# Optimization experiments

Hardware: AMD Instinct MI355X
Metric: run time of the kernel (lower is better)

## Reference

```python
import jax, jax.numpy as jnp
import numpy as np

EMBED_DIM = 768
NUM_HEADS = 12
HEAD_DIM = EMBED_DIM // NUM_HEADS  # 64
NUM_LEVELS = 2
Q_INDEX = (0, 6, 12)  # head-axis split per level
K_INDEX = (0, 6, 12)
V_INDEX = (0, 6, 12)


def setup_inputs() -> dict:
    key = jax.random.key(0)
    ks = jax.random.split(key, 12)
    std = 0.02
    d = {
        'inp0': jax.random.normal(ks[0], (8, 2048, 768), jnp.float32),
        'inp1': jax.random.normal(ks[1], (8, 1024, 1536), jnp.float32),
        'attn_mask': jax.random.normal(ks[2], (8, HEAD_DIM), jnp.float32),
        'Wq0': jax.random.normal(ks[3], (768, 768), jnp.float32) * std,
        'bq0': jnp.zeros((768,), jnp.float32),
        'Wk0': jax.random.normal(ks[4], (768, 768), jnp.float32) * std,
        'bk0': jnp.zeros((768,), jnp.float32),
        'Wv0': jax.random.normal(ks[5], (768, 768), jnp.float32) * std,
        'bv0': jnp.zeros((768,), jnp.float32),
        'Wq1': jax.random.normal(ks[6], (1536, 768), jnp.float32) * std,
        'bq1': jnp.zeros((768,), jnp.float32),
        'Wk1': jax.random.normal(ks[7], (1536, 768), jnp.float32) * std,
        'bk1': jnp.zeros((768,), jnp.float32),
        'Wv1': jax.random.normal(ks[8], (1536, 768), jnp.float32) * std,
        'bv1': jnp.zeros((768,), jnp.float32),
        'Wo': jax.random.normal(ks[9], (2 * 768, 768), jnp.float32) * std,
        'bo': jnp.zeros((768,), jnp.float32),
    }
    return d


def _split_heads(x):
    b, n, _ = x.shape
    return x.reshape(b, n, NUM_HEADS, HEAD_DIM).transpose(0, 2, 1, 3)  # b h n d


def _level_attention(level, inp, Wq, bq, Wk, bk, Wv, bv, attn_mask):
    q = _split_heads(inp @ Wq + bq)[:, Q_INDEX[level]:Q_INDEX[level + 1]]
    k = _split_heads(inp @ Wk + bk)[:, K_INDEX[level]:K_INDEX[level + 1]]
    v = _split_heads(inp @ Wv + bv)[:, V_INDEX[level]:V_INDEX[level + 1]]
    q = q * (HEAD_DIM ** -0.5)
    q = q + attn_mask[:, None, None, :]  # broadcast mask over heads & positions
    scores = jnp.einsum('bhnd,bhmd->bhnm', q, k)
    attn = jax.nn.softmax(scores, axis=-1)
    return jnp.einsum('bhnm,bhmd->bhnd', attn, v)  # b h n d


def reference(inp0, inp1, attn_mask, Wq0, bq0, Wk0, bk0, Wv0, bv0,
              Wq1, bq1, Wk1, bk1, Wv1, bv1, Wo, bo):
    levels = [
        (inp0, Wq0, bq0, Wk0, bk0, Wv0, bv0),
        (inp1, Wq1, bq1, Wk1, bk1, Wv1, bv1),
    ]
    outputs = [_level_attention(l, *args, attn_mask) for l, args in enumerate(levels)]
    n_max = max(o.shape[2] for o in outputs)
    merged, masks = [], []
    for o in outputs:
        b, h, n, dd = o.shape
        x = o.transpose(0, 2, 1, 3).reshape(b, n, h * dd)  # b n (h d)
        x = jnp.pad(x, ((0, 0), (0, n_max - n), (0, EMBED_DIM - h * dd)))
        merged.append(x)
        masks.append(jnp.pad(jnp.ones((n,), jnp.float32), (0, n_max - n)))
    x = jnp.concatenate(merged, axis=-1)  # [b, n_max, NUM_LEVELS*EMBED_DIM]
    output_mask = jnp.stack(masks)  # [NUM_LEVELS, n_max]
    output = x @ Wo + bo
    return (output, output_mask)
```

## Files before the change

### kernel.cpp

```cpp
#include <hip/hip_runtime.h>
#include <cmath>

typedef __bf16 bf16x8 __attribute__((ext_vector_type(8)));
typedef float floatx4 __attribute__((ext_vector_type(4)));

typedef __attribute__((address_space(1))) const void* as1_cvp;
typedef __attribute__((address_space(3))) void* as3_vp;

__device__ __forceinline__ void stage16(const void* g, void* l) {
    __builtin_amdgcn_global_load_lds((as1_cvp)g, (as3_vp)l, 16, 0, 0);
}

__global__ void conv_bf16(const float* __restrict__ in, __bf16* __restrict__ out, int n8)
{
    int t = blockIdx.x * 256 + threadIdx.x;
    if (t < n8) {
        floatx4 f0 = *(const floatx4*)&in[(size_t)t * 8];
        floatx4 f1 = *(const floatx4*)&in[(size_t)t * 8 + 4];
        bf16x8 o;
#pragma unroll
        for (int j = 0; j < 4; j++) { o[j] = (__bf16)f0[j]; o[4 + j] = (__bf16)f1[j]; }
        *(bf16x8*)&out[(size_t)t * 8] = o;
    }
}

__global__ void pack_qkv(const float* __restrict__ Wq, const float* __restrict__ Wk,
                         const float* __restrict__ Wv, __bf16* __restrict__ WT,
                         int Kd, int off)
{
    __shared__ __bf16 tile[64][72];
    int k0 = blockIdx.x * 64, c0 = blockIdx.y * 64;
    int proj = c0 / 384;
    const float* src = (proj == 0) ? Wq : (proj == 1) ? Wk : Wv;
    int lane = threadIdx.x & 63;
    int col = off + (c0 % 384) + lane;
    int tr = threadIdx.x >> 6;
#pragma unroll
    for (int i = 0; i < 16; i++) {
        int r = i * 4 + tr;
        tile[lane][r] = (__bf16)src[(size_t)(k0 + r) * 768 + col];
    }
    __syncthreads();
#pragma unroll
    for (int i = 0; i < 16; i++) {
        int cl = i * 4 + tr;
        WT[(size_t)(c0 + cl) * Kd + k0 + lane] = tile[cl][lane];
    }
}

__global__ void pack_wo(const float* __restrict__ Wo, __bf16* __restrict__ WT)
{
    __shared__ __bf16 tile[64][72];
    int k0 = blockIdx.x * 64, c0 = blockIdx.y * 64;
    int lane = threadIdx.x & 63;
    int col = c0 + lane;
    int tr = threadIdx.x >> 6;
#pragma unroll
    for (int i = 0; i < 16; i++) {
        int k = k0 + i * 4 + tr;
        int srow = k + (k >= 384 ? 384 : 0);
        tile[lane][i * 4 + tr] = (__bf16)Wo[(size_t)srow * 768 + col];
    }
    __syncthreads();
#pragma unroll
    for (int i = 0; i < 16; i++) {
        int cl = i * 4 + tr;
        WT[(size_t)(c0 + cl) * 768 + k0 + lane] = tile[cl][lane];
    }
}

__global__ __launch_bounds__(256, 2) void qkv_gemm(
    const __bf16* __restrict__ A, const __bf16* __restrict__ BT,
    const float* __restrict__ bq, const float* __restrict__ bk,
    const float* __restrict__ bv, const float* __restrict__ mask,
    __bf16* __restrict__ Qo, __bf16* __restrict__ Ko, __bf16* __restrict__ VTo,
    int Kd, int Nl, int nlsh, int off)
{
    __shared__ __bf16 As[128 * 64];
    __shared__ __bf16 Bs[128 * 64];
    const int tid = threadIdx.x;
    const int lane = tid & 63;
    const int wave = tid >> 6;
    const int lr = lane & 15, lg = lane >> 4;
    const int col0 = blockIdx.x * 128, row0 = blockIdx.y * 128;
    const int qr = (wave >> 1) * 64, qc = (wave & 1) * 64;
    floatx4 acc[4][4] = {};

    for (int k0 = 0; k0 < Kd; k0 += 64) {
        const __bf16* ga = A + (size_t)(row0 + wave * 32 + (lane >> 3)) * Kd + k0 + (lane & 7) * 8;
        const __bf16* gb = BT + (size_t)(col0 + wave * 32 + (lane >> 3)) * Kd + k0 + (lane & 7) * 8;
#pragma unroll
        for (int i = 0; i < 4; i++) {
            stage16(ga + (size_t)i * 8 * Kd, &As[(wave * 32 + i * 8) * 64]);
            stage16(gb + (size_t)i * 8 * Kd, &Bs[(wave * 32 + i * 8) * 64]);
        }
        __syncthreads();
#pragma unroll
        for (int ch = 0; ch < 2; ch++) {
            bf16x8 af[4], bfr[4];
#pragma unroll
            for (int mt = 0; mt < 4; mt++)
                af[mt] = *(const bf16x8*)&As[(qr + mt * 16 + lr) * 64 + ch * 32 + lg * 8];
#pragma unroll
            for (int nt = 0; nt < 4; nt++)
                bfr[nt] = *(const bf16x8*)&Bs[(qc + nt * 16 + lr) * 64 + ch * 32 + lg * 8];
#pragma unroll
            for (int mt = 0; mt < 4; mt++)
#pragma unroll
                for (int nt = 0; nt < 4; nt++)
                    acc[mt][nt] = __builtin_amdgcn_mfma_f32_16x16x32_bf16(af[mt], bfr[nt], acc[mt][nt], 0, 0, 0);
        }
        __syncthreads();
    }

    const float S_Q = 0.125f * 1.44269504088896f;
    const float S_M = 1.44269504088896f;
#pragma unroll
    for (int nt = 0; nt < 4; nt++) {
        int C = col0 + qc + nt * 16 + lr;
        int proj = C / 384;
        int rem = C - proj * 384;
        int h = rem >> 6, d = C & 63;
        float bias = (proj == 0) ? bq[off + rem]
                   : (proj == 1) ? bk[off + rem]
                                 : bv[off + rem];
#pragma unroll
        for (int mt = 0; mt < 4; mt++) {
#pragma unroll
            for (int r = 0; r < 4; r++) {
                int R = row0 + qr + mt * 16 + lg * 4 + r;
                int b = R >> nlsh;
                int n = R & (Nl - 1);
                size_t hb = (size_t)(b * 6 + h);
                float v = acc[mt][nt][r] + bias;
                if (proj == 0) {
                    v = fmaf(v, S_Q, S_M * mask[(b << 6) + d]);
                    Qo[(hb * Nl + n) * 64 + d] = (__bf16)v;
                } else if (proj == 1) {
                    Ko[(hb * Nl + n) * 64 + d] = (__bf16)v;
                } else {
                    VTo[(hb * 64 + d) * (size_t)Nl + n] = (__bf16)v;
                }
            }
        }
    }
}

__global__ __launch_bounds__(256, 4) void attn_kernel(
    const __bf16* __restrict__ Q, const __bf16* __restrict__ K,
    const __bf16* __restrict__ VT, __bf16* __restrict__ X,
    int Nl, int xoff)
{
    __shared__ __bf16 Ks[64 * 72];
    __shared__ __bf16 Vs[64 * 72];
    __shared__ __bf16 Ps[4][32 * 72];
    const int tid = threadIdx.x;
    const int wave = tid >> 6, lane = tid & 63;
    const int lr = lane & 15, lg = lane >> 4;
    const int h = blockIdx.y, b = blockIdx.z;
    const size_t head = (size_t)(b * 6 + h) * Nl * 64;
    const int q0 = blockIdx.x * 128 + wave * 16;

    bf16x8 qf[2][2];
#pragma unroll
    for (int s = 0; s < 2; s++)
#pragma unroll
        for (int ch = 0; ch < 2; ch++)
            qf[s][ch] = *(const bf16x8*)&Q[head + (size_t)(q0 + s * 64 + lr) * 64 + ch * 32 + lg * 8];

    bf16x8 onesv;
#pragma unroll
    for (int j = 0; j < 8; j++) onesv[j] = (__bf16)1.0f;

    const int rr = tid >> 2, cc = (tid & 3) * 16;
    const __bf16* Kg = K + head;
    const __bf16* Vg = VT + head;

    bf16x8 kr0, kr1, vr0, vr1;
    {
        size_t kb = (size_t)rr * 64 + cc;
        kr0 = *(const bf16x8*)&Kg[kb];
        kr1 = *(const bf16x8*)&Kg[kb + 8];
        size_t vb = (size_t)rr * Nl + cc;
        vr0 = *(const bf16x8*)&Vg[vb];
        vr1 = *(const bf16x8*)&Vg[vb + 8];
    }

    floatx4 o_acc[2][4] = {};
    floatx4 l_acc[2] = {};

    for (int n0 = 0; n0 < Nl; n0 += 64) {
        __syncthreads();
        *(bf16x8*)&Ks[rr * 72 + cc]     = kr0;
        *(bf16x8*)&Ks[rr * 72 + cc + 8] = kr1;
        *(bf16x8*)&Vs[rr * 72 + cc]     = vr0;
        *(bf16x8*)&Vs[rr * 72 + cc + 8] = vr1;
        __syncthreads();

        if (n0 + 64 < Nl) {
            size_t kb = (size_t)(n0 + 64 + rr) * 64 + cc;
            kr0 = *(const bf16x8*)&Kg[kb];
            kr1 = *(const bf16x8*)&Kg[kb + 8];
            size_t vb = (size_t)rr * Nl + n0 + 64 + cc;
            vr0 = *(const bf16x8*)&Vg[vb];
            vr1 = *(const bf16x8*)&Vg[vb + 8];
        }

        floatx4 sv[2][4] = {};
#pragma unroll
        for (int ch = 0; ch < 2; ch++) {
#pragma unroll
            for (int nt = 0; nt < 4; nt++) {
                bf16x8 kb8 = *(const bf16x8*)&Ks[(nt * 16 + lr) * 72 + ch * 32 + lg * 8];
                sv[0][nt] = __builtin_amdgcn_mfma_f32_16x16x32_bf16(qf[0][ch], kb8, sv[0][nt], 0, 0, 0);
                sv[1][nt] = __builtin_amdgcn_mfma_f32_16x16x32_bf16(qf[1][ch], kb8, sv[1][nt], 0, 0, 0);
            }
        }

#pragma unroll
        for (int s = 0; s < 2; s++)
#pragma unroll
            for (int nt = 0; nt < 4; nt++)
#pragma unroll
                for (int r = 0; r < 4; r++) {
                    float p = __builtin_amdgcn_exp2f(sv[s][nt][r]);
                    Ps[wave][(s * 16 + lg * 4 + r) * 72 + nt * 16 + lr] = (__bf16)p;
                }
        asm volatile("s_waitcnt lgkmcnt(0)" ::: "memory");

#pragma unroll
        for (int ch = 0; ch < 2; ch++) {
            bf16x8 pa0 = *(const bf16x8*)&Ps[wave][lr * 72 + ch * 32 + lg * 8];
            bf16x8 pa1 = *(const bf16x8*)&Ps[wave][(16 + lr) * 72 + ch * 32 + lg * 8];
#pragma unroll
            for (int dt = 0; dt < 4; dt++) {
                bf16x8 vb8 = *(const bf16x8*)&Vs[(dt * 16 + lr) * 72 + ch * 32 + lg * 8];
                o_acc[0][dt] = __builtin_amdgcn_mfma_f32_16x16x32_bf16(pa0, vb8, o_acc[0][dt], 0, 0, 0);
                o_acc[1][dt] = __builtin_amdgcn_mfma_f32_16x16x32_bf16(pa1, vb8, o_acc[1][dt], 0, 0, 0);
            }
            l_acc[0] = __builtin_amdgcn_mfma_f32_16x16x32_bf16(pa0, onesv, l_acc[0], 0, 0, 0);
            l_acc[1] = __builtin_amdgcn_mfma_f32_16x16x32_bf16(pa1, onesv, l_acc[1], 0, 0, 0);
        }
    }

#pragma unroll
    for (int s = 0; s < 2; s++)
#pragma unroll
        for (int dt = 0; dt < 4; dt++)
#pragma unroll
            for (int r = 0; r < 4; r++) {
                int n = q0 + s * 64 + lg * 4 + r;
                float o = o_acc[s][dt][r] / l_acc[s][r];
                X[(size_t)(b * 2048 + n) * 768 + xoff + h * 64 + dt * 16 + lr] = (__bf16)o;
            }
}

__global__ void fill_pad(__bf16* __restrict__ X, float* __restrict__ om)
{
    int t = blockIdx.x * 256 + threadIdx.x;
    if (t < 393216) {
        int r = t / 48;
        int c = (t - r * 48) * 8;
        int b = r >> 10, n = 1024 + (r & 1023);
        floatx4 z = {0.f, 0.f, 0.f, 0.f};
        *(floatx4*)&X[(size_t)(b * 2048 + n) * 768 + 384 + c] = z;
    }
    if (t < 4096) {
        om[t] = (t < 2048) ? 1.0f : (((t - 2048) < 1024) ? 1.0f : 0.0f);
    }
}

__global__ __launch_bounds__(256, 2) void out_gemm(
    const __bf16* __restrict__ A, const __bf16* __restrict__ BT,
    const float* __restrict__ bo, float* __restrict__ out)
{
    __shared__ __bf16 As[128 * 64];
    __shared__ __bf16 Bs[128 * 64];
    const int tid = threadIdx.x;
    const int lane = tid & 63;
    const int wave = tid >> 6;
    const int lr = lane & 15, lg = lane >> 4;
    const int col0 = blockIdx.x * 128, row0 = blockIdx.y * 128;
    const int qr = (wave >> 1) * 64, qc = (wave & 1) * 64;
    const int Kd = 768;
    floatx4 acc[4][4] = {};

    for (int k0 = 0; k0 < Kd; k0 += 64) {
        const __bf16* ga = A + (size_t)(row0 + wave * 32 + (lane >> 3)) * Kd + k0 + (lane & 7) * 8;
        const __bf16* gb = BT + (size_t)(col0 + wave * 32 + (lane >> 3)) * Kd + k0 + (lane & 7) * 8;
#pragma unroll
        for (int i = 0; i < 4; i++) {
            stage16(ga + (size_t)i * 8 * Kd, &As[(wave * 32 + i * 8) * 64]);
            stage16(gb + (size_t)i * 8 * Kd, &Bs[(wave * 32 + i * 8) * 64]);
        }
        __syncthreads();
#pragma unroll
        for (int ch = 0; ch < 2; ch++) {
            bf16x8 af[4], bfr[4];
#pragma unroll
            for (int mt = 0; mt < 4; mt++)
                af[mt] = *(const bf16x8*)&As[(qr + mt * 16 + lr) * 64 + ch * 32 + lg * 8];
#pragma unroll
            for (int nt = 0; nt < 4; nt++)
                bfr[nt] = *(const bf16x8*)&Bs[(qc + nt * 16 + lr) * 64 + ch * 32 + lg * 8];
#pragma unroll
            for (int mt = 0; mt < 4; mt++)
#pragma unroll
                for (int nt = 0; nt < 4; nt++)
                    acc[mt][nt] = __builtin_amdgcn_mfma_f32_16x16x32_bf16(af[mt], bfr[nt], acc[mt][nt], 0, 0, 0);
        }
        __syncthreads();
    }

#pragma unroll
    for (int nt = 0; nt < 4; nt++) {
        int C = col0 + qc + nt * 16 + lr;
        float bias = bo[C];
#pragma unroll
        for (int mt = 0; mt < 4; mt++) {
#pragma unroll
            for (int r = 0; r < 4; r++) {
                int R = row0 + qr + mt * 16 + lg * 4 + r;
                out[(size_t)R * 768 + C] = acc[mt][nt][r] + bias;
            }
        }
    }
}

extern "C" void kernel_launch(void* const* d_in, const int* in_sizes, int n_in,
                              void* d_out, int out_size, void* d_ws, size_t ws_size,
                              hipStream_t stream)
{
    const float* inp0  = (const float*)d_in[0];
    const float* inp1  = (const float*)d_in[1];
    const float* amask = (const float*)d_in[2];
    const float* Wq0 = (const float*)d_in[3];
    const float* bq0 = (const float*)d_in[4];
    const float* Wk0 = (const float*)d_in[5];
    const float* bk0 = (const float*)d_in[6];
    const float* Wv0 = (const float*)d_in[7];
    const float* bv0 = (const float*)d_in[8];
    const float* Wq1 = (const float*)d_in[9];
    const float* bq1 = (const float*)d_in[10];
    const float* Wk1 = (const float*)d_in[11];
    const float* bk1 = (const float*)d_in[12];
    const float* Wv1 = (const float*)d_in[13];
    const float* bv1 = (const float*)d_in[14];
    const float* Wo  = (const float*)d_in[15];
    const float* bo  = (const float*)d_in[16];

    char* ws = (char*)d_ws;
    __bf16* WT  = (__bf16*)(ws + 0);
    __bf16* WoT = (__bf16*)(ws + 3538944);
    __bf16* Ab  = (__bf16*)(ws + 4718592);
    __bf16* Qp  = (__bf16*)(ws + 29884416);
    __bf16* Kp  = (__bf16*)(ws + 42467328);
    __bf16* VT  = (__bf16*)(ws + 55050240);
    __bf16* X   = (__bf16*)(ws + 67633152);
    float* outp = (float*)d_out;

    hipLaunchKernelGGL(pack_wo, dim3(12, 12), dim3(256), 0, stream, Wo, WoT);

    hipLaunchKernelGGL(pack_qkv, dim3(12, 18), dim3(256), 0, stream, Wq0, Wk0, Wv0, WT, 768, 0);
    hipLaunchKernelGGL(conv_bf16, dim3(6144), dim3(256), 0, stream, inp0, Ab, 1572864);
    hipLaunchKernelGGL(qkv_gemm, dim3(9, 128), dim3(256), 0, stream,
                       Ab, WT, bq0, bk0, bv0, amask, Qp, Kp, VT, 768, 2048, 11, 0);
    hipLaunchKernelGGL(attn_kernel, dim3(16, 6, 8), dim3(256), 0, stream,
                       Qp, Kp, VT, X, 2048, 0);

    hipLaunchKernelGGL(pack_qkv, dim3(24, 18), dim3(256), 0, stream, Wq1, Wk1, Wv1, WT, 1536, 384);
    hipLaunchKernelGGL(conv_bf16, dim3(6144), dim3(256), 0, stream, inp1, Ab, 1572864);
    hipLaunchKernelGGL(qkv_gemm, dim3(9, 64), dim3(256), 0, stream,
                       Ab, WT, bq1, bk1, bv1, amask, Qp, Kp, VT, 1536, 1024, 10, 384);
    hipLaunchKernelGGL(attn_kernel, dim3(8, 6, 8), dim3(256), 0, stream,
                       Qp, Kp, VT, X, 1024, 384);

    hipLaunchKernelGGL(fill_pad, dim3(1536), dim3(256), 0, stream, X, outp + 12582912);
    hipLaunchKernelGGL(out_gemm, dim3(6, 128), dim3(256), 0, stream, X, WoT, bo, outp);
}
```

Baseline: 466.2 us.

## Merge per-level prep, QKV GEMM and attention launches into batched kernels

Replaces the eleven sequential launches with four: one prep kernel converts both inputs and packs all weight matrices, one QKV GEMM covers both levels through a flat block index, and one attention kernel covers both levels plus the padding fill. Each level gets separate Q/K/V and input buffers so the levels can run concurrently, and X aliases Ab0. The aim is to cut launch overhead and the tail underutilisation of small per-level grids. It costs more workspace, and the X/Ab0 aliasing depends on Ab0 no longer being read once qkv_all has finished.

```diff
diff --git a/kernel.cpp b/kernel.cpp
--- a/kernel.cpp
+++ b/kernel.cpp
@@ -11,78 +11,111 @@
     __builtin_amdgcn_global_load_lds((as1_cvp)g, (as3_vp)l, 16, 0, 0);
 }
 
-__global__ void conv_bf16(const float* __restrict__ in, __bf16* __restrict__ out, int n8)
+__global__ void prep_all(
+    const float* __restrict__ inp0, const float* __restrict__ inp1,
+    const float* __restrict__ Wq0, const float* __restrict__ Wk0, const float* __restrict__ Wv0,
+    const float* __restrict__ Wq1, const float* __restrict__ Wk1, const float* __restrict__ Wv1,
+    const float* __restrict__ Wo,
+    __bf16* __restrict__ Ab0, __bf16* __restrict__ Ab1,
+    __bf16* __restrict__ WT0, __bf16* __restrict__ WT1, __bf16* __restrict__ WoT)
 {
-    int t = blockIdx.x * 256 + threadIdx.x;
-    if (t < n8) {
+    __shared__ __bf16 tile[64][72];
+    const int bx = blockIdx.x;
+    const int tid = threadIdx.x;
+
+    if (bx < 12288) {
+        const float* in  = (bx < 6144) ? inp0 : inp1;
+        __bf16*      out = (bx < 6144) ? Ab0  : Ab1;
+        int t = (bx < 6144 ? bx : bx - 6144) * 256 + tid;
         floatx4 f0 = *(const floatx4*)&in[(size_t)t * 8];
         floatx4 f1 = *(const floatx4*)&in[(size_t)t * 8 + 4];
         bf16x8 o;
 #pragma unroll
         for (int j = 0; j < 4; j++) { o[j] = (__bf16)f0[j]; o[4 + j] = (__bf16)f1[j]; }
         *(bf16x8*)&out[(size_t)t * 8] = o;
-    }
-}
-
-__global__ void pack_qkv(const float* __restrict__ Wq, const float* __restrict__ Wk,
-                         const float* __restrict__ Wv, __bf16* __restrict__ WT,
-                         int Kd, int off)
-{
-    __shared__ __bf16 tile[64][72];
-    int k0 = blockIdx.x * 64, c0 = blockIdx.y * 64;
-    int proj = c0 / 384;
-    const float* src = (proj == 0) ? Wq : (proj == 1) ? Wk : Wv;
-    int lane = threadIdx.x & 63;
-    int col = off + (c0 % 384) + lane;
-    int tr = threadIdx.x >> 6;
-#pragma unroll
-    for (int i = 0; i < 16; i++) {
-        int r = i * 4 + tr;
-        tile[lane][r] = (__bf16)src[(size_t)(k0 + r) * 768 + col];
-    }
-    __syncthreads();
-#pragma unroll
-    for (int i = 0; i < 16; i++) {
-        int cl = i * 4 + tr;
-        WT[(size_t)(c0 + cl) * Kd + k0 + lane] = tile[cl][lane];
-    }
-}
-
-__global__ void pack_wo(const float* __restrict__ Wo, __bf16* __restrict__ WT)
-{
-    __shared__ __bf16 tile[64][72];
-    int k0 = blockIdx.x * 64, c0 = blockIdx.y * 64;
-    int lane = threadIdx.x & 63;
-    int col = c0 + lane;
-    int tr = threadIdx.x >> 6;
-#pragma unroll
-    for (int i = 0; i < 16; i++) {
-        int k = k0 + i * 4 + tr;
-        int srow = k + (k >= 384 ? 384 : 0);
-        tile[lane][i * 4 + tr] = (__bf16)Wo[(size_t)srow * 768 + col];
-    }
-    __syncthreads();
-#pragma unroll
-    for (int i = 0; i < 16; i++) {
-        int cl = i * 4 + tr;
-        WT[(size_t)(c0 + cl) * 768 + k0 + lane] = tile[cl][lane];
-    }
-}
-
-__global__ __launch_bounds__(256, 2) void qkv_gemm(
-    const __bf16* __restrict__ A, const __bf16* __restrict__ BT,
-    const float* __restrict__ bq, const float* __restrict__ bk,
-    const float* __restrict__ bv, const float* __restrict__ mask,
-    __bf16* __restrict__ Qo, __bf16* __restrict__ Ko, __bf16* __restrict__ VTo,
-    int Kd, int Nl, int nlsh, int off)
+        return;
+    }
+
+    int lane = tid & 63, tr = tid >> 6;
+
+    if (bx < 12936) {
+        int seg1 = (bx >= 12504);
+        int idx = seg1 ? bx - 12504 : bx - 12288;
+        int nkb = seg1 ? 24 : 12;
+        int Kd  = seg1 ? 1536 : 768;
+        int off = seg1 ? 384 : 0;
+        int k0 = (idx % nkb) * 64, c0 = (idx / nkb) * 64;
+        int proj = c0 / 384;
+        const float* src = seg1 ? ((proj == 0) ? Wq1 : (proj == 1) ? Wk1 : Wv1)
+                                : ((proj == 0) ? Wq0 : (proj == 1) ? Wk0 : Wv0);
+        __bf16* WT = seg1 ? WT1 : WT0;
+        int col = off + (c0 % 384) + lane;
+#pragma unroll
+        for (int i = 0; i < 16; i++) {
+            int r = i * 4 + tr;
+            tile[lane][r] = (__bf16)src[(size_t)(k0 + r) * 768 + col];
+        }
+        __syncthreads();
+#pragma unroll
+        for (int i = 0; i < 16; i++) {
+            int cl = i * 4 + tr;
+            WT[(size_t)(c0 + cl) * Kd + k0 + lane] = tile[cl][lane];
+        }
+        return;
+    }
+
+    {
+        int idx = bx - 12936;
+        int k0 = (idx % 12) * 64, c0 = (idx / 12) * 64;
+        int col = c0 + lane;
+#pragma unroll
+        for (int i = 0; i < 16; i++) {
+            int k = k0 + i * 4 + tr;
+            int srow = k + (k >= 384 ? 384 : 0);
+            tile[lane][i * 4 + tr] = (__bf16)Wo[(size_t)srow * 768 + col];
+        }
+        __syncthreads();
+#pragma unroll
+        for (int i = 0; i < 16; i++) {
+            int cl = i * 4 + tr;
+            WoT[(size_t)(c0 + cl) * 768 + k0 + lane] = tile[cl][lane];
+        }
+        return;
+    }
+}
+
+__global__ __launch_bounds__(256, 2) void qkv_all(
+    const __bf16* __restrict__ Ab0, const __bf16* __restrict__ Ab1,
+    const __bf16* __restrict__ WT0, const __bf16* __restrict__ WT1,
+    const float* __restrict__ bq0, const float* __restrict__ bk0, const float* __restrict__ bv0,
+    const float* __restrict__ bq1, const float* __restrict__ bk1, const float* __restrict__ bv1,
+    const float* __restrict__ mask,
+    __bf16* __restrict__ Q0, __bf16* __restrict__ K0, __bf16* __restrict__ V0T,
+    __bf16* __restrict__ Q1, __bf16* __restrict__ K1, __bf16* __restrict__ V1T)
 {
     __shared__ __bf16 As[128 * 64];
     __shared__ __bf16 Bs[128 * 64];
+    const int bx = blockIdx.x;
+    const int seg = (bx >= 1152);
+    const int idx = seg ? bx - 1152 : bx;
+    const int Kd  = seg ? 1536 : 768;
+    const int Nl  = seg ? 1024 : 2048;
+    const int nlsh = seg ? 10 : 11;
+    const int off = seg ? 384 : 0;
+    const __bf16* A  = seg ? Ab1 : Ab0;
+    const __bf16* BT = seg ? WT1 : WT0;
+    const float* bq = seg ? bq1 : bq0;
+    const float* bk = seg ? bk1 : bk0;
+    const float* bv = seg ? bv1 : bv0;
+    __bf16* Qo  = seg ? Q1 : Q0;
+    __bf16* Ko  = seg ? K1 : K0;
+    __bf16* VTo = seg ? V1T : V0T;
+
     const int tid = threadIdx.x;
     const int lane = tid & 63;
     const int wave = tid >> 6;
     const int lr = lane & 15, lg = lane >> 4;
-    const int col0 = blockIdx.x * 128, row0 = blockIdx.y * 128;
+    const int col0 = (idx % 9) * 128, row0 = (idx / 9) * 128;
     const int qr = (wave >> 1) * 64, qc = (wave & 1) * 64;
     floatx4 acc[4][4] = {};
 
@@ -146,20 +179,44 @@
     }
 }
 
-__global__ __launch_bounds__(256, 4) void attn_kernel(
-    const __bf16* __restrict__ Q, const __bf16* __restrict__ K,
-    const __bf16* __restrict__ VT, __bf16* __restrict__ X,
-    int Nl, int xoff)
+__global__ __launch_bounds__(256, 4) void attn_all(
+    const __bf16* __restrict__ Q0, const __bf16* __restrict__ K0, const __bf16* __restrict__ V0T,
+    const __bf16* __restrict__ Q1, const __bf16* __restrict__ K1, const __bf16* __restrict__ V1T,
+    __bf16* __restrict__ X, float* __restrict__ om)
 {
     __shared__ __bf16 Ks[64 * 72];
     __shared__ __bf16 Vs[64 * 72];
     __shared__ __bf16 Ps[4][32 * 72];
+    const int bx = blockIdx.x;
     const int tid = threadIdx.x;
+
+    if (bx >= 1152) {
+        int t = (bx - 1152) * 256 + tid;
+        int r = t / 48;
+        int c = (t - r * 48) * 8;
+        int b = r >> 10, n = 1024 + (r & 1023);
+        floatx4 z = {0.f, 0.f, 0.f, 0.f};
+        *(floatx4*)&X[(size_t)(b * 2048 + n) * 768 + 384 + c] = z;
+        if (t < 4096)
+            om[t] = (t < 2048) ? 1.0f : (((t - 2048) < 1024) ? 1.0f : 0.0f);
+        return;
+    }
+
+    const int seg = (bx >= 768);
+    const int idx = seg ? bx - 768 : bx;
+    const int Nl = seg ? 1024 : 2048;
+    const int qb = seg ? (idx & 7) : (idx & 15);
+    const int rest = seg ? (idx >> 3) : (idx >> 4);
+    const int h = rest % 6, b = rest / 6;
+    const int xoff = seg ? 384 : 0;
+    const __bf16* Q  = seg ? Q1 : Q0;
+    const __bf16* K  = seg ? K1 : K0;
+    const __bf16* VT = seg ? V1T : V0T;
+
     const int wave = tid >> 6, lane = tid & 63;
     const int lr = lane & 15, lg = lane >> 4;
-    const int h = blockIdx.y, b = blockIdx.z;
     const size_t head = (size_t)(b * 6 + h) * Nl * 64;
-    const int q0 = blockIdx.x * 128 + wave * 16;
+    const int q0 = qb * 128 + wave * 16;
 
     bf16x8 qf[2][2];
 #pragma unroll
@@ -253,21 +310,6 @@
                 float o = o_acc[s][dt][r] / l_acc[s][r];
                 X[(size_t)(b * 2048 + n) * 768 + xoff + h * 64 + dt * 16 + lr] = (__bf16)o;
             }
-}
-
-__global__ void fill_pad(__bf16* __restrict__ X, float* __restrict__ om)
-{
-    int t = blockIdx.x * 256 + threadIdx.x;
-    if (t < 393216) {
-        int r = t / 48;
-        int c = (t - r * 48) * 8;
-        int b = r >> 10, n = 1024 + (r & 1023);
-        floatx4 z = {0.f, 0.f, 0.f, 0.f};
-        *(floatx4*)&X[(size_t)(b * 2048 + n) * 768 + 384 + c] = z;
-    }
-    if (t < 4096) {
-        om[t] = (t < 2048) ? 1.0f : (((t - 2048) < 1024) ? 1.0f : 0.0f);
-    }
 }
 
 __global__ __launch_bounds__(256, 2) void out_gemm(
@@ -350,31 +392,29 @@
     const float* bo  = (const float*)d_in[16];
 
     char* ws = (char*)d_ws;
-    __bf16* WT  = (__bf16*)(ws + 0);
-    __bf16* WoT = (__bf16*)(ws + 3538944);
-    __bf16* Ab  = (__bf16*)(ws + 4718592);
-    __bf16* Qp  = (__bf16*)(ws + 29884416);
-    __bf16* Kp  = (__bf16*)(ws + 42467328);
-    __bf16* VT  = (__bf16*)(ws + 55050240);
-    __bf16* X   = (__bf16*)(ws + 67633152);
+    __bf16* WT0 = (__bf16*)(ws + 0);
+    __bf16* WT1 = (__bf16*)(ws + 1769472);
+    __bf16* WoT = (__bf16*)(ws + 5308416);
+    __bf16* Ab0 = (__bf16*)(ws + 6488064);
+    __bf16* X   = Ab0;
+    __bf16* Ab1 = (__bf16*)(ws + 31653888);
+    __bf16* Q0  = (__bf16*)(ws + 56819712);
+    __bf16* K0  = (__bf16*)(ws + 69402624);
+    __bf16* V0T = (__bf16*)(ws + 81985536);
+    __bf16* Q1  = (__bf16*)(ws + 94568448);
+    __bf16* K1  = (__bf16*)(ws + 100859904);
+    __bf16* V1T = (__bf16*)(ws + 107151360);
     float* outp = (float*)d_out;
 
-    hipLaunchKernelGGL(pack_wo, dim3(12, 12), dim3(256), 0, stream, Wo, WoT);
-
-    hipLaunchKernelGGL(pack_qkv, dim3(12, 18), dim3(256), 0, stream, Wq0, Wk0, Wv0, WT, 768, 0);
-    hipLaunchKernelGGL(conv_bf16, dim3(6144), dim3(256), 0, stream, inp0, Ab, 1572864);
-    hipLaunchKernelGGL(qkv_gemm, dim3(9, 128), dim3(256), 0, stream,
-                       Ab, WT, bq0, bk0, bv0, amask, Qp, Kp, VT, 768, 2048, 11, 0);
-    hipLaunchKernelGGL(attn_kernel, dim3(16, 6, 8), dim3(256), 0, stream,
-                       Qp, Kp, VT, X, 2048, 0);
-
-    hipLaunchKernelGGL(pack_qkv, dim3(24, 18), dim3(256), 0, stream, Wq1, Wk1, Wv1, WT, 1536, 384);
-    hipLaunchKernelGGL(conv_bf16, dim3(6144), dim3(256), 0, stream, inp1, Ab, 1572864);
-    hipLaunchKernelGGL(qkv_gemm, dim3(9, 64), dim3(256), 0, stream,
-                       Ab, WT, bq1, bk1, bv1, amask, Qp, Kp, VT, 1536, 1024, 10, 384);
-    hipLaunchKernelGGL(attn_kernel, dim3(8, 6, 8), dim3(256), 0, stream,
-                       Qp, Kp, VT, X, 1024, 384);
-
-    hipLaunchKernelGGL(fill_pad, dim3(1536), dim3(256), 0, stream, X, outp + 12582912);
-    hipLaunchKernelGGL(out_gemm, dim3(6, 128), dim3(256), 0, stream, X, WoT, bo, outp);
-}
+    hipLaunchKernelGGL(prep_all, dim3(13080), dim3(256), 0, stream,
+                       inp0, inp1, Wq0, Wk0, Wv0, Wq1, Wk1, Wv1, Wo,
+                       Ab0, Ab1, WT0, WT1, WoT);
+    hipLaunchKernelGGL(qkv_all, dim3(1728), dim3(256), 0, stream,
+                       Ab0, Ab1, WT0, WT1,
+                       bq0, bk0, bv0, bq1, bk1, bv1, amask,
+                       Q0, K0, V0T, Q1, K1, V1T);
+    hipLaunchKernelGGL(attn_all, dim3(2688), dim3(256), 0, stream,
+                       Q0, K0, V0T, Q1, K1, V1T, X, outp + 12582912);
+    hipLaunchKernelGGL(out_gemm, dim3(6, 128), dim3(256), 0, stream,
+                       X, WoT, bo, outp);
+}
```

After: 440.4 us. 5.5% less time.
